# Kernel optimization log

Measured on AMD Instinct MI355X. Metric: run time of the kernel, lower is better.

## Reference

```python
import jax, jax.numpy as jnp
import numpy as np

N = 100000
E = 3200000
IN_DIM = 256
HID = 128
HID2 = 64
K = 16


def setup_inputs() -> dict:
    key = jax.random.key(0)
    ks = jax.random.split(key, 12)
    x = jax.random.normal(ks[0], (N, IN_DIM), dtype=jnp.float32)
    edge_index = jax.random.randint(ks[1], (2, E), 0, N, dtype=jnp.int64)
    edge_weight = jax.random.uniform(ks[2], (E,), dtype=jnp.float32)
    s = lambda f: 1.0 / np.sqrt(f)
    W0 = jax.random.normal(ks[3], (IN_DIM, HID), dtype=jnp.float32) * s(IN_DIM)
    b0 = jnp.zeros((HID,), jnp.float32)
    P0w = jax.random.normal(ks[4], (IN_DIM, HID), dtype=jnp.float32) * s(IN_DIM)
    P0b = jnp.zeros((HID,), jnp.float32)
    W1 = jax.random.normal(ks[5], (HID, HID2), dtype=jnp.float32) * s(HID)
    b1 = jnp.zeros((HID2,), jnp.float32)
    P1w = jax.random.normal(ks[6], (HID, HID2), dtype=jnp.float32) * s(HID)
    P1b = jnp.zeros((HID2,), jnp.float32)
    W2 = jax.random.normal(ks[7], (HID2, K), dtype=jnp.float32) * s(HID2)
    b2 = jnp.zeros((K,), jnp.float32)
    return {"x": x, "edge_index": edge_index, "edge_weight": edge_weight,
            "W0": W0, "b0": b0, "P0w": P0w, "P0b": P0b,
            "W1": W1, "b1": b1, "P1w": P1w, "P1b": P1b,
            "W2": W2, "b2": b2}


def _gcn_norm(edge_index, edge_weight, n):
    # add self loops (weight 1), symmetric normalization per PyG gcn_norm
    loop = jnp.arange(n, dtype=edge_index.dtype)
    row = jnp.concatenate([edge_index[0], loop])
    col = jnp.concatenate([edge_index[1], loop])
    w = jnp.concatenate([edge_weight, jnp.ones((n,), edge_weight.dtype)])
    deg = jax.ops.segment_sum(w, col, num_segments=n)
    dinv = jnp.where(deg > 0, jax.lax.rsqrt(deg), 0.0)
    return row, col, dinv[row] * w * dinv[col]


def reference(x, edge_index, edge_weight, W0, b0, P0w, P0b, W1, b1, P1w, P1b, W2, b2):
    n = x.shape[0]
    row, col, nw = _gcn_norm(edge_index, edge_weight, n)

    def gcn(h, W, b):
        hW = h @ W  # transform first (PyG GCNConv), then scatter-aggregate
        agg = jax.ops.segment_sum(nw[:, None] * hW[row], col, num_segments=n)
        return agg + b

    # layer 0: skip is Linear(input_dim, hidden); dropout = identity (eval)
    h = jax.nn.selu(gcn(x, W0, b0) + (x @ P0w + P0b))
    # layer 1: skip is Linear(hidden, hidden//2)
    h = jax.nn.selu(gcn(h, W1, b1) + (h @ P1w + P1b))
    # layer 2: no skip, no dropout
    h = jax.nn.selu(gcn(h, W2, b2))
    return jax.nn.softmax(h, axis=-1)
```

## Files before the change

### kernel.cpp

```cpp
#include <hip/hip_runtime.h>
#include <hip/hip_fp16.h>
#include <cmath>

#define IN_DIM 256
#define HID 128
#define HID2 64
#define SB 512
#define NODES_PB 256
#define NBKT_MAX 448
#define BCAP 9216
#define CHB 3328
#define CH 4096
#define SMEM_BIN (4 * NBKT_MAX * 4 + CHB * 9)

struct __align__(8) EdgeP { int s; float w; };
union H4 { __half h[4]; uint2 u; };
union H2 { __half2 h2; uint u; };

using f16x8 = __attribute__((ext_vector_type(8))) _Float16;
using f32x4 = __attribute__((ext_vector_type(4))) float;

__device__ __forceinline__ float selu_f(float x) {
    const float scale = 1.0507009873554805f;
    const float alpha = 1.6732632423543772f;
    return x > 0.f ? scale * x : scale * alpha * expm1f(x);
}


__global__ void zero_ints(int* p, int n) {
    int i = blockIdx.x * blockDim.x + threadIdx.x;
    if (i < n) p[i] = 0;
}

__global__ void transpose_w(const float* __restrict__ B1, const float* __restrict__ B2,
                            __half* __restrict__ WT, int K, int C1, int C2) {
    int c = blockIdx.x;
    for (int k = threadIdx.x; k < K; k += blockDim.x) {
        float v = (c < C1) ? B1[(size_t)k * C1 + c] : B2[(size_t)k * C2 + (c - C1)];
        WT[(size_t)c * K + k] = __float2half(v);
    }
}

__global__ void deg_dinv(const EdgeP* __restrict__ ell, int* cnt, float* dinv, int n, int cap) {
    int wid = (blockIdx.x * blockDim.x + threadIdx.x) >> 6;
    int lane = threadIdx.x & 63;
    if (wid >= n) return;
    size_t base = (size_t)wid * cap;
    int len = min(cnt[wid], cap);
    float s = 0.f;
    for (int i = lane; i < len; i += 64) s += ell[base + i].w;
#pragma unroll
    for (int o = 32; o; o >>= 1) s += __shfl_xor(s, o);
    if (lane == 0) {
        dinv[wid] = rsqrtf(s + 1.0f);
        cnt[wid] = len;
    }
}

template <int PER>
__device__ __forceinline__ void wave0_excl_scan(const int* lds_in, int* lds_out, int nb, int tid) {
    if (tid < 64) {
        int r[PER];
        int sum = 0;
#pragma unroll
        for (int k = 0; k < PER; ++k) {
            int idx = tid * PER + k;
            int v = (idx < nb) ? lds_in[idx] : 0;
            r[k] = sum;
            sum += v;
        }
        int run = sum;
#pragma unroll
        for (int o = 1; o < 64; o <<= 1) {
            int t = __shfl_up(run, o);
            if (tid >= o) run += t;
        }
        int excl = run - sum;
#pragma unroll
        for (int k = 0; k < PER; ++k) {
            int idx = tid * PER + k;
            if (idx < nb) lds_out[idx] = excl + r[k];
        }
    }
}

__global__ __launch_bounds__(256) void bin_gemm0(
    const float* __restrict__ A, const __half* __restrict__ WT,
    const float* __restrict__ bias1, const float* __restrict__ bias2,
    __half* __restrict__ outA, float* __restrict__ outB, int M,
    const int* __restrict__ ei, const float* __restrict__ ew,
    int* cnt_or_bcur, EdgeP* __restrict__ dst_buf,
    int E, int cap, int epb, int sblocks, int nb, int mode) {
    const int tid = threadIdx.x;
    __shared__ __align__(16) char smem[SMEM_BIN];

    if ((int)blockIdx.x < sblocks) {
        int lo = blockIdx.x * epb;
        int hi = min(E, lo + epb);
        if (mode == 1) {
            int* gwcur = (int*)smem;
            int* chist = gwcur + NBKT_MAX;
            int* coff = chist + NBKT_MAX;
            int* ccur = coff + NBKT_MAX;
            int* sortedS = ccur + NBKT_MAX;
            float* sortedW = (float*)(sortedS + CHB);
            unsigned char* smap = (unsigned char*)(sortedW + CHB);

            for (int i = tid; i < nb; i += 256) chist[i] = 0;
            __syncthreads();
            for (int e0 = lo; e0 < hi; e0 += 2048) {
                int d[8];
#pragma unroll
                for (int j = 0; j < 8; ++j) {
                    int e = e0 + j * 256 + tid;
                    d[j] = (e < hi) ? ei[E + e] : -1;
                }
#pragma unroll
                for (int j = 0; j < 8; ++j)
                    if (d[j] >= 0) atomicAdd(&chist[d[j] >> 8], 1);
            }
            __syncthreads();
            for (int b = tid; b < nb; b += 256) {
                int h = chist[b];
                gwcur[b] = h ? atomicAdd(&cnt_or_bcur[b], h) : 0;
            }
            __syncthreads();

            for (int c0 = lo; c0 < hi; c0 += CHB) {
                int cn = min(CHB, hi - c0);
                for (int i = tid; i < nb; i += 256) chist[i] = 0;
                __syncthreads();
                for (int r0 = 0; r0 < cn; r0 += 2048) {
                    int d[8];
#pragma unroll
                    for (int j = 0; j < 8; ++j) {
                        int r = r0 + j * 256 + tid;
                        d[j] = (r < cn) ? ei[E + c0 + r] : -1;
                    }
#pragma unroll
                    for (int j = 0; j < 8; ++j)
                        if (d[j] >= 0) atomicAdd(&chist[d[j] >> 8], 1);
                }
                __syncthreads();
                wave0_excl_scan<7>(chist, coff, nb, tid);
                __syncthreads();
                for (int b = tid; b < nb; b += 256) ccur[b] = coff[b];
                __syncthreads();
                for (int r0 = 0; r0 < cn; r0 += 2048) {
                    int d[8], s8[8];
                    float w8[8];
#pragma unroll
                    for (int j = 0; j < 8; ++j) {
                        int r = r0 + j * 256 + tid;
                        d[j] = -1;
                        if (r < cn) {
                            int e = c0 + r;
                            d[j] = ei[E + e];
                            s8[j] = ei[e];
                            w8[j] = ew[e];
                        }
                    }
#pragma unroll
                    for (int j = 0; j < 8; ++j)
                        if (d[j] >= 0) {
                            int b = d[j] >> 8;
                            int slot = atomicAdd(&ccur[b], 1);
                            sortedS[slot] = (s8[j] << 8) | (d[j] & 255) | ((b >> 8) << 25);
                            sortedW[slot] = w8[j];
                            smap[slot] = (unsigned char)(b & 255);
                        }
                }
                __syncthreads();
                for (int i0 = 0; i0 < cn; i0 += 2048) {
                    int key[8], bb[8];
                    float wv[8];
#pragma unroll
                    for (int j = 0; j < 8; ++j) {
                        int i = i0 + j * 256 + tid;
                        bb[j] = -1;
                        if (i < cn) {
                            key[j] = sortedS[i];
                            wv[j] = sortedW[i];
                            bb[j] = smap[i] | (((key[j] >> 25) & 1) << 8);
                        }
                    }
#pragma unroll
                    for (int j = 0; j < 8; ++j)
                        if (bb[j] >= 0) {
                            int i = i0 + j * 256 + tid;
                            int addr = gwcur[bb[j]] + (i - coff[bb[j]]);
                            if (addr < BCAP) {
                                EdgeP p; p.s = key[j] & 0x01FFFFFF; p.w = wv[j];
                                dst_buf[(size_t)bb[j] * BCAP + addr] = p;
                            }
                        }
                }
                __syncthreads();
                for (int b = tid; b < nb; b += 256) gwcur[b] += chist[b];
                __syncthreads();
            }
        } else {
            for (int base = lo; base < hi; base += 2048) {
                int r[8], c[8], pos[8];
                float wv[8];
#pragma unroll
                for (int j = 0; j < 8; ++j) {
                    int e = base + j * 256 + tid;
                    c[j] = -1;
                    if (e < hi) { r[j] = ei[e]; c[j] = ei[E + e]; wv[j] = ew[e]; }
                }
#pragma unroll
                for (int j = 0; j < 8; ++j)
                    if (c[j] >= 0) pos[j] = atomicAdd(&cnt_or_bcur[c[j]], 1);
#pragma unroll
                for (int j = 0; j < 8; ++j)
                    if (c[j] >= 0 && pos[j] < cap) {
                        EdgeP p; p.s = r[j]; p.w = wv[j];
                        dst_buf[(size_t)c[j] * cap + pos[j]] = p;
                    }
            }
        }
        return;
    }

    __half* sA16 = (__half*)smem;
    __half* sB16 = (__half*)(smem + 10240);
    const int bid = blockIdx.x - sblocks;
    const int m0 = (bid >> 1) * 128;
    const int n0 = (bid & 1) * 128;
    const int lane = tid & 63;
    const int wv = tid >> 6;
    const int wr = (wv >> 1) * 64;
    const int wc = (wv & 1) * 64;
    const int lr = lane & 15, lk = lane >> 4;

    f32x4 zero = {0.f, 0.f, 0.f, 0.f};
    f32x4 acc[4][4];
#pragma unroll
    for (int i = 0; i < 4; ++i)
#pragma unroll
        for (int j = 0; j < 4; ++j) acc[i][j] = zero;

    for (int k0 = 0; k0 < IN_DIM; k0 += 32) {
#pragma unroll
        for (int p = 0; p < 4; ++p) {
            int f4 = p * 256 + tid;
            int r = f4 >> 3;
            int kk = (f4 & 7) << 2;
            int row = m0 + r;
            float4 v = make_float4(0.f, 0.f, 0.f, 0.f);
            if (row < M) v = *(const float4*)(A + (size_t)row * IN_DIM + k0 + kk);
            H4 h;
            h.h[0] = __float2half(v.x); h.h[1] = __float2half(v.y);
            h.h[2] = __float2half(v.z); h.h[3] = __float2half(v.w);
            *(uint2*)&sA16[r * 40 + kk] = h.u;
        }
#pragma unroll
        for (int p = 0; p < 2; ++p) {
            int f = p * 256 + tid;
            int c = f >> 2;
            int kc = (f & 3) << 3;
            *(uint4*)&sB16[c * 40 + kc] =
                *(const uint4*)(WT + (size_t)(n0 + c) * IN_DIM + k0 + kc);
        }
        __syncthreads();
        f16x8 af[4], bf[4];
#pragma unroll
        for (int i = 0; i < 4; ++i)
            af[i] = *(const f16x8*)&sA16[(wr + i * 16 + lr) * 40 + lk * 8];
#pragma unroll
        for (int j = 0; j < 4; ++j)
            bf[j] = *(const f16x8*)&sB16[(wc + j * 16 + lr) * 40 + lk * 8];
#pragma unroll
        for (int i = 0; i < 4; ++i)
#pragma unroll
            for (int j = 0; j < 4; ++j)
                acc[i][j] = __builtin_amdgcn_mfma_f32_16x16x32_f16(af[i], bf[j], acc[i][j], 0, 0, 0);
        __syncthreads();
    }

    float bs[4];
    if (n0 != 0) {
#pragma unroll
        for (int j = 0; j < 4; ++j) {
            int c = wc + j * 16 + lr;
            bs[j] = bias1[c] + bias2[c];
        }
    }
#pragma unroll
    for (int i = 0; i < 4; ++i) {
        int rowb = m0 + wr + i * 16 + lk * 4;
#pragma unroll
        for (int j = 0; j < 4; ++j) {
            int col = wc + j * 16 + lr;
#pragma unroll
            for (int r = 0; r < 4; ++r) {
                int row = rowb + r;
                if (row < M) {
                    if (n0 == 0)
                        outA[(size_t)row * HID + col] = __float2half(acc[i][j][r]);
                    else
                        outB[(size_t)row * HID + col] = acc[i][j][r] + bs[j];
                }
            }
        }
    }
}

__global__ __launch_bounds__(256) void bucket_build(
    const EdgeP* __restrict__ recs, const int* __restrict__ bcur,
    EdgeP* __restrict__ ell, int* __restrict__ cnt, float* __restrict__ dinv,
    int n, int cap) {
    __shared__ int lcnt[NODES_PB];
    __shared__ float ldeg[NODES_PB];
    __shared__ int chist[NODES_PB];
    __shared__ int coff[NODES_PB];
    __shared__ int ccur[NODES_PB];
    __shared__ __align__(8) int sortedS[CH];
    __shared__ float sortedW[CH];
    __shared__ unsigned char cmap[CH];
    int b = blockIdx.x, tid = threadIdx.x;
    lcnt[tid] = 0;
    ldeg[tid] = 0.f;
    __syncthreads();
    int m = min(bcur[b], BCAP);
    const EdgeP* rbase = recs + (size_t)b * BCAP;
    for (int c0 = 0; c0 < m; c0 += CH) {
        int cn = min(CH, m - c0);
        chist[tid] = 0;
        __syncthreads();
        for (int i0 = 0; i0 < cn; i0 += 2048) {
            EdgeP p[8];
            int ok[8];
#pragma unroll
            for (int j = 0; j < 8; ++j) {
                int i = i0 + j * 256 + tid;
                ok[j] = (i < cn);
                if (ok[j]) p[j] = rbase[c0 + i];
            }
#pragma unroll
            for (int j = 0; j < 8; ++j)
                if (ok[j]) {
                    int dl = p[j].s & 255;
                    atomicAdd(&chist[dl], 1);
                    atomicAdd(&ldeg[dl], p[j].w);
                }
        }
        __syncthreads();
        wave0_excl_scan<4>(chist, coff, NODES_PB, tid);
        __syncthreads();
        ccur[tid] = coff[tid];
        __syncthreads();
        for (int i0 = 0; i0 < cn; i0 += 2048) {
            EdgeP p[8];
            int ok[8];
#pragma unroll
            for (int j = 0; j < 8; ++j) {
                int i = i0 + j * 256 + tid;
                ok[j] = (i < cn);
                if (ok[j]) p[j] = rbase[c0 + i];
            }
#pragma unroll
            for (int j = 0; j < 8; ++j)
                if (ok[j]) {
                    int dl = p[j].s & 255;
                    int slot = atomicAdd(&ccur[dl], 1);
                    sortedS[slot] = p[j].s >> 8;
                    sortedW[slot] = p[j].w;
                    cmap[slot] = (unsigned char)dl;
                }
        }
        __syncthreads();
        for (int i0 = 0; i0 < cn; i0 += 2048) {
            int s8[8], dl8[8];
            float w8[8];
#pragma unroll
            for (int j = 0; j < 8; ++j) {
                int i = i0 + j * 256 + tid;
                dl8[j] = -1;
                if (i < cn) {
                    s8[j] = sortedS[i];
                    w8[j] = sortedW[i];
                    dl8[j] = cmap[i];
                }
            }
#pragma unroll
            for (int j = 0; j < 8; ++j)
                if (dl8[j] >= 0) {
                    int i = i0 + j * 256 + tid;
                    int rank = lcnt[dl8[j]] + (i - coff[dl8[j]]);
                    if (rank < cap) {
                        EdgeP q; q.s = s8[j]; q.w = w8[j];
                        ell[((size_t)(b * NODES_PB + dl8[j])) * cap + rank] = q;
                    }
                }
        }
        __syncthreads();
        lcnt[tid] += chist[tid];
        __syncthreads();
    }
    int v = b * NODES_PB + tid;
    if (v < n) {
        cnt[v] = min(lcnt[tid], cap);
        dinv[v] = rsqrtf(ldeg[tid] + 1.0f);
    }
}

__global__ __launch_bounds__(256) void gemm1_fused(
    const float* __restrict__ A, const __half* __restrict__ WT,
    const float* __restrict__ bias1, const float* __restrict__ bias2,
    __half* __restrict__ outA, float* __restrict__ outB, int M) {
    const int tid = threadIdx.x;
    __shared__ __align__(16) __half sA16[128 * 40];
    __shared__ __align__(16) __half sB16[128 * 40];
    const int m0 = blockIdx.x * 128;
    const int lane = tid & 63;
    const int wv = tid >> 6;
    const int wr = (wv >> 1) * 64;
    const int wc = (wv & 1) * 64;
    const int lr = lane & 15, lk = lane >> 4;

    f32x4 zero = {0.f, 0.f, 0.f, 0.f};
    f32x4 acc[4][4];
#pragma unroll
    for (int i = 0; i < 4; ++i)
#pragma unroll
        for (int j = 0; j < 4; ++j) acc[i][j] = zero;

    for (int k0 = 0; k0 < HID; k0 += 32) {
#pragma unroll
        for (int p = 0; p < 4; ++p) {
            int f4 = p * 256 + tid;
            int r = f4 >> 3;
            int kk = (f4 & 7) << 2;
            int row = m0 + r;
            float4 v = make_float4(0.f, 0.f, 0.f, 0.f);
            if (row < M) v = *(const float4*)(A + (size_t)row * HID + k0 + kk);
            H4 h;
            h.h[0] = __float2half(v.x); h.h[1] = __float2half(v.y);
            h.h[2] = __float2half(v.z); h.h[3] = __float2half(v.w);
            *(uint2*)&sA16[r * 40 + kk] = h.u;
        }
#pragma unroll
        for (int p = 0; p < 2; ++p) {
            int f = p * 256 + tid;
            int c = f >> 2;
            int kc = (f & 3) << 3;
            *(uint4*)&sB16[c * 40 + kc] =
                *(const uint4*)(WT + (size_t)c * HID + k0 + kc);
        }
        __syncthreads();
        f16x8 af[4], bf[4];
#pragma unroll
        for (int i = 0; i < 4; ++i)
            af[i] = *(const f16x8*)&sA16[(wr + i * 16 + lr) * 40 + lk * 8];
#pragma unroll
        for (int j = 0; j < 4; ++j)
            bf[j] = *(const f16x8*)&sB16[(wc + j * 16 + lr) * 40 + lk * 8];
#pragma unroll
        for (int i = 0; i < 4; ++i)
#pragma unroll
            for (int j = 0; j < 4; ++j)
                acc[i][j] = __builtin_amdgcn_mfma_f32_16x16x32_f16(af[i], bf[j], acc[i][j], 0, 0, 0);
        __syncthreads();
    }

    float bs[4];
    if (wc != 0) {
#pragma unroll
        for (int j = 0; j < 4; ++j) {
            int c = wc + j * 16 + lr - HID2;
            bs[j] = bias1[c] + bias2[c];
        }
    }
#pragma unroll
    for (int i = 0; i < 4; ++i) {
        int rowb = m0 + wr + i * 16 + lk * 4;
#pragma unroll
        for (int j = 0; j < 4; ++j) {
            int col = wc + j * 16 + lr;
#pragma unroll
            for (int r = 0; r < 4; ++r) {
                int row = rowb + r;
                if (row < M) {
                    if (wc == 0)
                        outA[(size_t)row * HID2 + col] = __float2half(acc[i][j][r]);
                    else
                        outB[(size_t)row * HID2 + (col - HID2)] = acc[i][j][r] + bs[j];
                }
            }
        }
    }
}

__global__ __launch_bounds__(256) void aggregate128(
    const __half* __restrict__ hW, float* __restrict__ S,
    const float* __restrict__ dinv, const int* __restrict__ cnt,
    const EdgeP* __restrict__ ell, int cap, int n) {
    int v = (blockIdx.x * 256 + threadIdx.x) >> 6;
    int lane = threadIdx.x & 63;
    if (v >= n) return;
    float di = dinv[v];
    float2 sv = *(const float2*)&S[(size_t)v * HID + lane * 2];
    H2 selfh; selfh.u = *(const uint*)&hW[(size_t)v * HID + lane * 2];
    float2 selff = __half22float2(selfh.h2);
    float selfx = sv.x + di * di * selff.x;
    float selfy = sv.y + di * di * selff.y;

    size_t base = (size_t)v * cap;
    int len = cnt[v];
    float ax[4] = {0.f, 0.f, 0.f, 0.f};
    float ay[4] = {0.f, 0.f, 0.f, 0.f};
    int i = 0;
    for (; i + 8 <= len; i += 8) {
        EdgeP p[8];
        float dv[8];
        uint h[8];
#pragma unroll
        for (int j = 0; j < 8; ++j) p[j] = ell[base + i + j];
#pragma unroll
        for (int j = 0; j < 8; ++j) {
            dv[j] = dinv[p[j].s];
            h[j] = *(const uint*)&hW[(size_t)p[j].s * HID + lane * 2];
        }
#pragma unroll
        for (int j = 0; j < 8; ++j) {
            float t = dv[j] * p[j].w;
            H2 hh; hh.u = h[j];
            float2 hf = __half22float2(hh.h2);
            ax[j & 3] = fmaf(t, hf.x, ax[j & 3]);
            ay[j & 3] = fmaf(t, hf.y, ay[j & 3]);
        }
    }
    for (; i < len; ++i) {
        EdgeP p = ell[base + i];
        float t = dinv[p.s] * p.w;
        H2 hh; hh.u = *(const uint*)&hW[(size_t)p.s * HID + lane * 2];
        float2 hf = __half22float2(hh.h2);
        ax[0] = fmaf(t, hf.x, ax[0]);
        ay[0] = fmaf(t, hf.y, ay[0]);
    }
    float sx = selfx + di * ((ax[0] + ax[1]) + (ax[2] + ax[3]));
    float sy = selfy + di * ((ay[0] + ay[1]) + (ay[2] + ay[3]));
    *(float2*)&S[(size_t)v * HID + lane * 2] = make_float2(selu_f(sx), selu_f(sy));
}

__global__ __launch_bounds__(256) void agg64_gemm2(
    const __half* __restrict__ hW, const float* __restrict__ S,
    const float* __restrict__ dinv, const int* __restrict__ cnt,
    const EdgeP* __restrict__ ell, int cap,
    const float* __restrict__ W2, __half* __restrict__ out16, int n) {
    __shared__ float sW[64 * 16];
    __shared__ float sh[4][64];
    int tid = threadIdx.x;
#pragma unroll
    for (int i = 0; i < 4; ++i) sW[i * 256 + tid] = W2[i * 256 + tid];

    int g = tid >> 6, f = tid & 63;
    int v = blockIdx.x * 4 + g;
    if (v < n) {
        float di = dinv[v];
        float self = S[(size_t)v * 64 + f] + di * di * __half2float(hW[(size_t)v * 64 + f]);
        size_t base = (size_t)v * cap;
        int len = cnt[v];
        float a[4] = {0.f, 0.f, 0.f, 0.f};
        int i = 0;
        for (; i + 8 <= len; i += 8) {
            EdgeP p[8];
            float dv[8];
            __half hv[8];
#pragma unroll
            for (int j = 0; j < 8; ++j) p[j] = ell[base + i + j];
#pragma unroll
            for (int j = 0; j < 8; ++j) {
                dv[j] = dinv[p[j].s];
                hv[j] = hW[(size_t)p[j].s * 64 + f];
            }
#pragma unroll
            for (int j = 0; j < 8; ++j)
                a[j & 3] = fmaf(dv[j] * p[j].w, __half2float(hv[j]), a[j & 3]);
        }
        for (; i < len; ++i) {
            EdgeP p = ell[base + i];
            a[0] = fmaf(dinv[p.s] * p.w, __half2float(hW[(size_t)p.s * 64 + f]), a[0]);
        }
        sh[g][f] = selu_f(self + di * ((a[0] + a[1]) + (a[2] + a[3])));
    }
    __syncthreads();
    if (v < n && f < 16) {
        float acc = 0.f;
#pragma unroll
        for (int k = 0; k < 64; ++k) acc = fmaf(sh[g][k], sW[k * 16 + f], acc);
        out16[(size_t)v * 16 + f] = __float2half(acc);
    }
}

__global__ __launch_bounds__(256) void agg_softmax(
    const __half* __restrict__ hW, const float* __restrict__ b2,
    const float* __restrict__ dinv, const int* __restrict__ cnt,
    const EdgeP* __restrict__ ell, int cap,
    float* __restrict__ out, int n) {
    int tid = threadIdx.x;
    int g = tid >> 4, f = tid & 15;
    int v = blockIdx.x * 16 + g;
    if (v >= n) return;
    float di = dinv[v];
    float acc = b2[f] + di * di * __half2float(hW[(size_t)v * 16 + f]);
    size_t base = (size_t)v * cap;
    int len = cnt[v];
    float a[4] = {0.f, 0.f, 0.f, 0.f};
    int i = 0;
    for (; i + 4 <= len; i += 4) {
        EdgeP p[4];
        float dv[4];
        __half hv[4];
#pragma unroll
        for (int j = 0; j < 4; ++j) p[j] = ell[base + i + j];
#pragma unroll
        for (int j = 0; j < 4; ++j) {
            dv[j] = dinv[p[j].s];
            hv[j] = hW[(size_t)p[j].s * 16 + f];
        }
#pragma unroll
        for (int j = 0; j < 4; ++j)
            a[j] = fmaf(dv[j] * p[j].w, __half2float(hv[j]), a[j]);
    }
    for (; i < len; ++i) {
        EdgeP p = ell[base + i];
        a[0] = fmaf(dinv[p.s] * p.w, __half2float(hW[(size_t)p.s * 16 + f]), a[0]);
    }
    acc += di * ((a[0] + a[1]) + (a[2] + a[3]));
    acc = selu_f(acc);
    float m = acc;
    m = fmaxf(m, __shfl_xor(m, 1));
    m = fmaxf(m, __shfl_xor(m, 2));
    m = fmaxf(m, __shfl_xor(m, 4));
    m = fmaxf(m, __shfl_xor(m, 8));
    float ex = expf(acc - m);
    float sm = ex;
    sm += __shfl_xor(sm, 1);
    sm += __shfl_xor(sm, 2);
    sm += __shfl_xor(sm, 4);
    sm += __shfl_xor(sm, 8);
    out[(size_t)v * 16 + f] = ex / sm;
}

extern "C" void kernel_launch(void* const* d_in, const int* in_sizes, int n_in,
                              void* d_out, int out_size, void* d_ws, size_t ws_size,
                              hipStream_t stream) {
    const float* x = (const float*)d_in[0];
    const int* ei = (const int*)d_in[1];
    const float* ew = (const float*)d_in[2];
    const float* W0 = (const float*)d_in[3];
    const float* b0 = (const float*)d_in[4];
    const float* P0w = (const float*)d_in[5];
    const float* P0b = (const float*)d_in[6];
    const float* W1 = (const float*)d_in[7];
    const float* b1 = (const float*)d_in[8];
    const float* P1w = (const float*)d_in[9];
    const float* P1b = (const float*)d_in[10];
    const float* W2 = (const float*)d_in[11];
    const float* b2 = (const float*)d_in[12];
    float* out = (float*)d_out;
    const int n = in_sizes[0] / IN_DIM;
    const int E = in_sizes[2];
    const int NB = (n + NODES_PB - 1) / NODES_PB;

    auto al = [](size_t b) { return (b + 255) & ~(size_t)255; };
    size_t oCnt = 0;
    size_t oDinv = oCnt + al((size_t)n * 4);
    size_t oBcur = oDinv + al((size_t)n * 4);
    size_t oWT0 = oBcur + al((size_t)NBKT_MAX * 4);
    size_t oWT1 = oWT0 + al((size_t)IN_DIM * (HID * 2) * 2);
    size_t oA = oWT1 + al((size_t)HID * HID * 2);
    size_t oB = oA + al((size_t)n * HID * 2);
    size_t oEll = oB + al((size_t)n * HID * 4);
    size_t szEll96 = al((size_t)n * 96 * 8);
    size_t szEll80 = al((size_t)n * 80 * 8);
    size_t szRec = al((size_t)NB * BCAP * 8);
    size_t szCD = al((size_t)n * HID2 * 4) + al((size_t)n * 16 * 2);
    size_t szR = szRec > szCD ? szRec : szCD;

    int cap;
    int mode;
    if (NB <= NBKT_MAX && oEll + szEll96 + szR <= ws_size) { cap = 96; mode = 1; }
    else if (oEll + szEll96 + szCD <= ws_size) { cap = 96; mode = 0; }
    else { cap = 80; mode = 0; }

    char* base = (char*)d_ws;
    int* cnt = (int*)(base + oCnt);
    float* dinv = (float*)(base + oDinv);
    int* bcur = (int*)(base + oBcur);
    __half* WT0 = (__half*)(base + oWT0);
    __half* WT1 = (__half*)(base + oWT1);
    __half* bufA = (__half*)(base + oA);
    float* bufB = (float*)(base + oB);
    EdgeP* ell = (EdgeP*)(base + oEll);
    size_t oR = oEll + (cap == 96 ? szEll96 : szEll80);
    EdgeP* recs = (EdgeP*)(base + oR);
    float* bufC = (float*)(base + oR);
    __half* bufD = (__half*)(base + oR + al((size_t)n * HID2 * 4));

    int gx = (n + 127) / 128;
    int gemmBlocks = gx * 2;
    int epb = (E + SB - 1) / SB;

    transpose_w<<<2 * HID, 128, 0, stream>>>(W0, P0w, WT0, IN_DIM, HID, HID);
    transpose_w<<<HID, 128, 0, stream>>>(W1, P1w, WT1, HID, HID2, HID2);

    if (mode == 1) {
        zero_ints<<<(NBKT_MAX + 255) / 256, 256, 0, stream>>>(bcur, NBKT_MAX);
        bin_gemm0<<<SB + gemmBlocks, 256, 0, stream>>>(
            x, WT0, b0, P0b, bufA, bufB, n, ei, ew, bcur, recs,
            E, cap, epb, SB, NB, 1);
        bucket_build<<<NB, NODES_PB, 0, stream>>>(recs, bcur, ell, cnt, dinv, n, cap);
    } else {
        zero_ints<<<(n + 255) / 256, 256, 0, stream>>>(cnt, n);
        bin_gemm0<<<SB + gemmBlocks, 256, 0, stream>>>(
            x, WT0, b0, P0b, bufA, bufB, n, ei, ew, cnt, ell,
            E, cap, epb, SB, NB, 0);
        int nbW = (n * 64 + 255) / 256;
        deg_dinv<<<nbW, 256, 0, stream>>>(ell, cnt, dinv, n, cap);
    }

    aggregate128<<<(n * 64 + 255) / 256, 256, 0, stream>>>(bufA, bufB, dinv, cnt, ell, cap, n);

    gemm1_fused<<<gx, 256, 0, stream>>>(bufB, WT1, b1, P1b, bufA, bufC, n);

    agg64_gemm2<<<(n + 3) / 4, 256, 0, stream>>>(bufA, bufC, dinv, cnt, ell, cap, W2, bufD, n);
    agg_softmax<<<(n + 15) / 16, 256, 0, stream>>>(bufD, b2, dinv, cnt, ell, cap, out, n);
}
```

Baseline: 487.5 us.

## Store skip/intermediate buffers in fp16 and unroll aggregation loops by 16

The skip-projection and aggregation output buffers (bufB, bufC) change from fp32 to fp16 storage across gemm0, aggregate128, gemm1 and agg64_gemm2. gemm1 now loads fp16 activations directly instead of converting fp32 on load. This halves the memory traffic for these intermediates. The aggregation kernels also gain a 16-wide unrolled gather loop to keep more loads in flight. The trade-off is lower precision in the intermediate skip and hidden activations, plus higher register pressure.

```diff
diff --git a/kernel.cpp b/kernel.cpp
--- a/kernel.cpp
+++ b/kernel.cpp
@@ -87,7 +87,7 @@
 __global__ __launch_bounds__(256) void bin_gemm0(
     const float* __restrict__ A, const __half* __restrict__ WT,
     const float* __restrict__ bias1, const float* __restrict__ bias2,
-    __half* __restrict__ outA, float* __restrict__ outB, int M,
+    __half* __restrict__ outA, __half* __restrict__ outB, int M,
     const int* __restrict__ ei, const float* __restrict__ ew,
     int* cnt_or_bcur, EdgeP* __restrict__ dst_buf,
     int E, int cap, int epb, int sblocks, int nb, int mode) {
@@ -279,14 +279,6 @@
         __syncthreads();
     }
 
-    float bs[4];
-    if (n0 != 0) {
-#pragma unroll
-        for (int j = 0; j < 4; ++j) {
-            int c = wc + j * 16 + lr;
-            bs[j] = bias1[c] + bias2[c];
-        }
-    }
 #pragma unroll
     for (int i = 0; i < 4; ++i) {
         int rowb = m0 + wr + i * 16 + lk * 4;
@@ -300,7 +292,8 @@
                     if (n0 == 0)
                         outA[(size_t)row * HID + col] = __float2half(acc[i][j][r]);
                     else
-                        outB[(size_t)row * HID + col] = acc[i][j][r] + bs[j];
+                        outB[(size_t)row * HID + col] =
+                            __float2half(acc[i][j][r] + bias1[col] + bias2[col]);
                 }
             }
         }
@@ -407,9 +400,9 @@
 }
 
 __global__ __launch_bounds__(256) void gemm1_fused(
-    const float* __restrict__ A, const __half* __restrict__ WT,
+    const __half* __restrict__ A, const __half* __restrict__ WT,
     const float* __restrict__ bias1, const float* __restrict__ bias2,
-    __half* __restrict__ outA, float* __restrict__ outB, int M) {
+    __half* __restrict__ outA, __half* __restrict__ outB, int M) {
     const int tid = threadIdx.x;
     __shared__ __align__(16) __half sA16[128 * 40];
     __shared__ __align__(16) __half sB16[128 * 40];
@@ -429,17 +422,14 @@
 
     for (int k0 = 0; k0 < HID; k0 += 32) {
 #pragma unroll
-        for (int p = 0; p < 4; ++p) {
-            int f4 = p * 256 + tid;
-            int r = f4 >> 3;
-            int kk = (f4 & 7) << 2;
+        for (int p = 0; p < 2; ++p) {
+            int f = p * 256 + tid;
+            int r = f >> 2;
+            int kc = (f & 3) << 3;
             int row = m0 + r;
-            float4 v = make_float4(0.f, 0.f, 0.f, 0.f);
-            if (row < M) v = *(const float4*)(A + (size_t)row * HID + k0 + kk);
-            H4 h;
-            h.h[0] = __float2half(v.x); h.h[1] = __float2half(v.y);
-            h.h[2] = __float2half(v.z); h.h[3] = __float2half(v.w);
-            *(uint2*)&sA16[r * 40 + kk] = h.u;
+            uint4 v = make_uint4(0, 0, 0, 0);
+            if (row < M) v = *(const uint4*)(A + (size_t)row * HID + k0 + kc);
+            *(uint4*)&sA16[r * 40 + kc] = v;
         }
 #pragma unroll
         for (int p = 0; p < 2; ++p) {
@@ -465,14 +455,6 @@
         __syncthreads();
     }
 
-    float bs[4];
-    if (wc != 0) {
-#pragma unroll
-        for (int j = 0; j < 4; ++j) {
-            int c = wc + j * 16 + lr - HID2;
-            bs[j] = bias1[c] + bias2[c];
-        }
-    }
 #pragma unroll
     for (int i = 0; i < 4; ++i) {
         int rowb = m0 + wr + i * 16 + lk * 4;
@@ -485,8 +467,11 @@
                 if (row < M) {
                     if (wc == 0)
                         outA[(size_t)row * HID2 + col] = __float2half(acc[i][j][r]);
-                    else
-                        outB[(size_t)row * HID2 + (col - HID2)] = acc[i][j][r] + bs[j];
+                    else {
+                        int c = col - HID2;
+                        outB[(size_t)row * HID2 + c] =
+                            __float2half(acc[i][j][r] + bias1[c] + bias2[c]);
+                    }
                 }
             }
         }
@@ -494,14 +479,15 @@
 }
 
 __global__ __launch_bounds__(256) void aggregate128(
-    const __half* __restrict__ hW, float* __restrict__ S,
+    const __half* __restrict__ hW, __half* __restrict__ S,
     const float* __restrict__ dinv, const int* __restrict__ cnt,
     const EdgeP* __restrict__ ell, int cap, int n) {
     int v = (blockIdx.x * 256 + threadIdx.x) >> 6;
     int lane = threadIdx.x & 63;
     if (v >= n) return;
     float di = dinv[v];
-    float2 sv = *(const float2*)&S[(size_t)v * HID + lane * 2];
+    H2 svh; svh.u = *(const uint*)&S[(size_t)v * HID + lane * 2];
+    float2 sv = __half22float2(svh.h2);
     H2 selfh; selfh.u = *(const uint*)&hW[(size_t)v * HID + lane * 2];
     float2 selff = __half22float2(selfh.h2);
     float selfx = sv.x + di * di * selff.x;
@@ -512,6 +498,26 @@
     float ax[4] = {0.f, 0.f, 0.f, 0.f};
     float ay[4] = {0.f, 0.f, 0.f, 0.f};
     int i = 0;
+    for (; i + 16 <= len; i += 16) {
+        EdgeP p[16];
+        float dv[16];
+        uint h[16];
+#pragma unroll
+        for (int j = 0; j < 16; ++j) p[j] = ell[base + i + j];
+#pragma unroll
+        for (int j = 0; j < 16; ++j) {
+            dv[j] = dinv[p[j].s];
+            h[j] = *(const uint*)&hW[(size_t)p[j].s * HID + lane * 2];
+        }
+#pragma unroll
+        for (int j = 0; j < 16; ++j) {
+            float t = dv[j] * p[j].w;
+            H2 hh; hh.u = h[j];
+            float2 hf = __half22float2(hh.h2);
+            ax[j & 3] = fmaf(t, hf.x, ax[j & 3]);
+            ay[j & 3] = fmaf(t, hf.y, ay[j & 3]);
+        }
+    }
     for (; i + 8 <= len; i += 8) {
         EdgeP p[8];
         float dv[8];
@@ -542,11 +548,14 @@
     }
     float sx = selfx + di * ((ax[0] + ax[1]) + (ax[2] + ax[3]));
     float sy = selfy + di * ((ay[0] + ay[1]) + (ay[2] + ay[3]));
-    *(float2*)&S[(size_t)v * HID + lane * 2] = make_float2(selu_f(sx), selu_f(sy));
+    H2 o;
+    o.h2.x = __float2half(selu_f(sx));
+    o.h2.y = __float2half(selu_f(sy));
+    *(uint*)&S[(size_t)v * HID + lane * 2] = o.u;
 }
 
 __global__ __launch_bounds__(256) void agg64_gemm2(
-    const __half* __restrict__ hW, const float* __restrict__ S,
+    const __half* __restrict__ hW, const __half* __restrict__ S,
     const float* __restrict__ dinv, const int* __restrict__ cnt,
     const EdgeP* __restrict__ ell, int cap,
     const float* __restrict__ W2, __half* __restrict__ out16, int n) {
@@ -560,11 +569,27 @@
     int v = blockIdx.x * 4 + g;
     if (v < n) {
         float di = dinv[v];
-        float self = S[(size_t)v * 64 + f] + di * di * __half2float(hW[(size_t)v * 64 + f]);
+        float self = __half2float(S[(size_t)v * 64 + f]) +
+                     di * di * __half2float(hW[(size_t)v * 64 + f]);
         size_t base = (size_t)v * cap;
         int len = cnt[v];
         float a[4] = {0.f, 0.f, 0.f, 0.f};
         int i = 0;
+        for (; i + 16 <= len; i += 16) {
+            EdgeP p[16];
+            float dv[16];
+            __half hv[16];
+#pragma unroll
+            for (int j = 0; j < 16; ++j) p[j] = ell[base + i + j];
+#pragma unroll
+            for (int j = 0; j < 16; ++j) {
+                dv[j] = dinv[p[j].s];
+                hv[j] = hW[(size_t)p[j].s * 64 + f];
+            }
+#pragma unroll
+            for (int j = 0; j < 16; ++j)
+                a[j & 3] = fmaf(dv[j] * p[j].w, __half2float(hv[j]), a[j & 3]);
+        }
         for (; i + 8 <= len; i += 8) {
             EdgeP p[8];
             float dv[8];
@@ -674,11 +699,11 @@
     size_t oWT1 = oWT0 + al((size_t)IN_DIM * (HID * 2) * 2);
     size_t oA = oWT1 + al((size_t)HID * HID * 2);
     size_t oB = oA + al((size_t)n * HID * 2);
-    size_t oEll = oB + al((size_t)n * HID * 4);
+    size_t oEll = oB + al((size_t)n * HID * 2);
     size_t szEll96 = al((size_t)n * 96 * 8);
     size_t szEll80 = al((size_t)n * 80 * 8);
     size_t szRec = al((size_t)NB * BCAP * 8);
-    size_t szCD = al((size_t)n * HID2 * 4) + al((size_t)n * 16 * 2);
+    size_t szCD = al((size_t)n * HID2 * 2) + al((size_t)n * 16 * 2);
     size_t szR = szRec > szCD ? szRec : szCD;
 
     int cap;
@@ -694,12 +719,12 @@
     __half* WT0 = (__half*)(base + oWT0);
     __half* WT1 = (__half*)(base + oWT1);
     __half* bufA = (__half*)(base + oA);
-    float* bufB = (float*)(base + oB);
+    __half* bufB = (__half*)(base + oB);
     EdgeP* ell = (EdgeP*)(base + oEll);
     size_t oR = oEll + (cap == 96 ? szEll96 : szEll80);
     EdgeP* recs = (EdgeP*)(base + oR);
-    float* bufC = (float*)(base + oR);
-    __half* bufD = (__half*)(base + oR + al((size_t)n * HID2 * 4));
+    __half* bufC = (__half*)(base + oR);
+    __half* bufD = (__half*)(base + oR + al((size_t)n * HID2 * 2));
 
     int gx = (n + 127) / 128;
     int gemmBlocks = gx * 2;
```

New measurement: 559.1 us. 14.7% more time.
